# Optimization experiments

Hardware: AMD Instinct MI355X
Metric: run time of the kernel (lower is better)

## Reference

```python
import jax, jax.numpy as jnp
import numpy as np

E = 8        # n_routed_experts
TOPK = 2     # num_experts_per_tok


def setup_inputs() -> dict:
    key = jax.random.key(0)
    k0, k1, k2, k3, k4 = jax.random.split(key, 5)
    B, S, D, H = 1, 2048, 1024, 2816
    scale = 0.02
    x = jax.random.normal(k0, (B, S, D), jnp.float32)
    Wg = jax.random.normal(k1, (E, D), jnp.float32) * scale   # gate weight [E, D]
    W1 = jax.random.normal(k2, (E, H, D), jnp.float32) * scale  # up-gate proj
    W2 = jax.random.normal(k3, (E, D, H), jnp.float32) * scale  # down proj
    W3 = jax.random.normal(k4, (E, H, D), jnp.float32) * scale  # up proj
    return {"x": x, "Wg": Wg, "W1": W1, "W2": W2, "W3": W3}


def _moe_forward(x, Wg, W1, W2, W3):
    B, S, D = x.shape
    xt = x.reshape(-1, D)                      # [T, D], T = B*S
    T = xt.shape[0]
    # --- gate: logits -> softmax -> top-k, normalized top-k weights ---
    logits = xt @ Wg.T                         # [T, E]
    scores = jax.nn.softmax(logits, axis=-1)
    w, idx = jax.lax.top_k(scores, TOPK)       # [T, K]
    w = w / (w.sum(axis=-1, keepdims=True) + 1e-20)
    # combine weights per token per expert (scatter top-k weights) [T, E]
    cw = jnp.zeros((T, E), xt.dtype).at[jnp.arange(T)[:, None], idx].add(w)
    # --- per-expert SwiGLU FFN (batched over experts) ---
    h = jax.nn.silu(jnp.einsum('td,ehd->teh', xt, W1)) * jnp.einsum('td,ehd->teh', xt, W3)  # [T,E,H]
    out = jnp.einsum('teh,edh->ted', h, W2)    # [T, E, D]
    # weighted combine of selected experts (cw is zero for unselected)
    y = jnp.einsum('te,ted->td', cw, out)      # [T, D]
    return y.reshape(B, S, D)


def reference(x, Wg, W1, W2, W3):
    return _moe_forward(x, Wg, W1, W2, W3)
```

## Files before the change

### kernel.cpp

```cpp
#include <hip/hip_runtime.h>
#include <hip/hip_bf16.h>

#define T_TOK 2048
#define D_DIM 1024
#define H_DIM 2816
#define E_NUM 8
#define NPOS  (2 * T_TOK)
#define SLACK 1024

typedef __attribute__((ext_vector_type(8))) short short8;
typedef __attribute__((ext_vector_type(4))) float floatx4;

__device__ __forceinline__ unsigned short f2bf(float f) {
    unsigned int b = __float_as_uint(f);
    b += 0x7FFFu + ((b >> 16) & 1u);
    return (unsigned short)(b >> 16);
}

__device__ __forceinline__ short8 pack8(float4 a, float4 b) {
    short8 o;
    o[0] = (short)f2bf(a.x); o[1] = (short)f2bf(a.y);
    o[2] = (short)f2bf(a.z); o[3] = (short)f2bf(a.w);
    o[4] = (short)f2bf(b.x); o[5] = (short)f2bf(b.y);
    o[6] = (short)f2bf(b.z); o[7] = (short)f2bf(b.w);
    return o;
}

__device__ __forceinline__ void gl2lds16(const void* g, void* l) {
    __builtin_amdgcn_global_load_lds(
        (const __attribute__((address_space(1))) unsigned int*)g,
        (__attribute__((address_space(3))) unsigned int*)l,
        16, 0, 0);
}


__global__ __launch_bounds__(256) void k_gate(const float* __restrict__ x,
                                              const float* __restrict__ Wg,
                                              int* __restrict__ topi, float* __restrict__ topw,
                                              int* __restrict__ counts) {
    int wave = threadIdx.x >> 6, lane = threadIdx.x & 63;
    int t = blockIdx.x * 4 + wave;
    const float* xr = x + (size_t)t * D_DIM;
    float acc[E_NUM];
#pragma unroll
    for (int e = 0; e < E_NUM; ++e) acc[e] = 0.f;
    for (int i = 0; i < D_DIM / 64; ++i) {
        float xv = xr[lane + 64 * i];
#pragma unroll
        for (int e = 0; e < E_NUM; ++e) acc[e] += xv * Wg[e * D_DIM + lane + 64 * i];
    }
#pragma unroll
    for (int e = 0; e < E_NUM; ++e) {
#pragma unroll
        for (int s = 32; s > 0; s >>= 1) acc[e] += __shfl_xor(acc[e], s, 64);
    }
    if (lane == 0) {
        float mx = acc[0];
#pragma unroll
        for (int e = 1; e < E_NUM; ++e) mx = fmaxf(mx, acc[e]);
        float p[E_NUM], s = 0.f;
#pragma unroll
        for (int e = 0; e < E_NUM; ++e) { p[e] = expf(acc[e] - mx); s += p[e]; }
        int i0 = 0;
#pragma unroll
        for (int e = 1; e < E_NUM; ++e) if (p[e] > p[i0]) i0 = e;
        int i1 = (i0 == 0) ? 1 : 0;
#pragma unroll
        for (int e = 0; e < E_NUM; ++e) if (e != i0 && p[e] > p[i1]) i1 = e;
        float s0 = p[i0] / s, s1 = p[i1] / s;
        float d = s0 + s1 + 1e-20f;
        topi[t * 2] = i0; topi[t * 2 + 1] = i1;
        topw[t * 2] = s0 / d; topw[t * 2 + 1] = s1 / d;
        atomicAdd(&counts[i0], 1);
        atomicAdd(&counts[i1], 1);
    }
}

__global__ void k_scan(const int* __restrict__ counts, int* __restrict__ offs,
                       int* __restrict__ cursor) {
    if (threadIdx.x == 0) {
        int s = 0;
        for (int e = 0; e < E_NUM; ++e) { offs[e] = s; cursor[e] = s; s += counts[e]; }
        offs[E_NUM] = s;
    }
}

__global__ __launch_bounds__(256) void k_scatter(const int* __restrict__ topi,
                                                 int* __restrict__ cursor,
                                                 int* __restrict__ ltok,
                                                 int* __restrict__ tpos) {
    int t = blockIdx.x * 256 + threadIdx.x;
#pragma unroll
    for (int k = 0; k < 2; ++k) {
        int e = topi[t * 2 + k];
        int pos = atomicAdd(&cursor[e], 1);
        ltok[pos] = t;
        tpos[t * 2 + k] = pos;
    }
}

__global__ __launch_bounds__(256) void k_gather(const float* __restrict__ x,
                                                const int* __restrict__ ltok,
                                                unsigned short* __restrict__ xg) {
    int p = blockIdx.x;
    int t = ltok[p];
    const float4* src = (const float4*)(x + (size_t)t * D_DIM);
    ushort4* dst = (ushort4*)(xg + (size_t)p * D_DIM);
    float4 v = src[threadIdx.x];
    ushort4 o;
    o.x = f2bf(v.x); o.y = f2bf(v.y); o.z = f2bf(v.z); o.w = f2bf(v.w);
    dst[threadIdx.x] = o;
}

__global__ __launch_bounds__(256) void k_gemm13(const unsigned short* __restrict__ xg,
                                                const float* __restrict__ W1,
                                                const float* __restrict__ W3,
                                                const int* __restrict__ offs,
                                                const int* __restrict__ counts,
                                                unsigned short* __restrict__ U) {
    const int nt = blockIdx.x;
    const int mt = blockIdx.y;
    const int e  = blockIdx.z;
    const int cnt = counts[e];
    if (mt * 256 >= cnt) return;
    const int off = offs[e];

    __shared__ __align__(16) unsigned char As[32 * 1056];
    __shared__ __align__(16) unsigned char B1s[4 * 1056];
    __shared__ __align__(16) unsigned char B3s[4 * 1056];

    const int tid = threadIdx.x, lane = tid & 63, wave = tid >> 6;
    const int fr = lane & 15, quad = lane >> 4, f7 = fr & 7, f8 = fr >> 3;

    const unsigned short* aBase = xg
        + ((size_t)off + mt * 256 + wave * 64 + (lane >> 3)) * D_DIM
        + ((lane & 7) ^ (lane >> 3)) * 8;

    const int br = tid >> 3, bc = tid & 7;
    const float* w1p = W1 + ((size_t)e * H_DIM + nt * 32 + br) * D_DIM + bc * 8;
    const float* w3p = W3 + ((size_t)e * H_DIM + nt * 32 + br) * D_DIM + bc * 8;
    const int bslot = (br >> 3) * 1056 + (br & 7) * 128 + ((bc ^ (br & 7)) << 4);

    floatx4 acc1[4][2], acc3[4][2];
#pragma unroll
    for (int m = 0; m < 4; ++m)
#pragma unroll
        for (int n = 0; n < 2; ++n) { acc1[m][n] = (floatx4)0.f; acc3[m][n] = (floatx4)0.f; }

    const int agrp = (wave * 8 + f8) * 1056 + f7 * 128;
    const int c0 = (quad ^ f7) << 4;
    const int c1 = ((4 | quad) ^ f7) << 4;

#pragma unroll 1
    for (int k0 = 0; k0 < D_DIM; k0 += 64) {
#pragma unroll
        for (int j = 0; j < 8; ++j)
            gl2lds16(aBase + (size_t)j * 8 * D_DIM + k0, As + (wave * 8 + j) * 1056);
        float4 u0 = *(const float4*)(w1p + k0);
        float4 u1 = *(const float4*)(w1p + k0 + 4);
        float4 v0 = *(const float4*)(w3p + k0);
        float4 v1 = *(const float4*)(w3p + k0 + 4);
        *(short8*)(B1s + bslot) = pack8(u0, u1);
        *(short8*)(B3s + bslot) = pack8(v0, v1);
        __syncthreads();

        short8 b1f[2][2], b3f[2][2];
#pragma unroll
        for (int n = 0; n < 2; ++n) {
            const int bg = (n * 2 + f8) * 1056 + f7 * 128;
            b1f[n][0] = *(const short8*)(B1s + bg + c0);
            b1f[n][1] = *(const short8*)(B1s + bg + c1);
            b3f[n][0] = *(const short8*)(B3s + bg + c0);
            b3f[n][1] = *(const short8*)(B3s + bg + c1);
        }
#pragma unroll
        for (int m = 0; m < 4; ++m) {
            const unsigned char* ab = As + agrp + m * 2112;
            short8 a0 = *(const short8*)(ab + c0);
            short8 a1 = *(const short8*)(ab + c1);
#pragma unroll
            for (int n = 0; n < 2; ++n) {
                acc1[m][n] = __builtin_amdgcn_mfma_f32_16x16x32_bf16(a0, b1f[n][0], acc1[m][n], 0, 0, 0);
                acc1[m][n] = __builtin_amdgcn_mfma_f32_16x16x32_bf16(a1, b1f[n][1], acc1[m][n], 0, 0, 0);
                acc3[m][n] = __builtin_amdgcn_mfma_f32_16x16x32_bf16(a0, b3f[n][0], acc3[m][n], 0, 0, 0);
                acc3[m][n] = __builtin_amdgcn_mfma_f32_16x16x32_bf16(a1, b3f[n][1], acc3[m][n], 0, 0, 0);
            }
        }
        __syncthreads();
    }

#pragma unroll
    for (int m = 0; m < 4; ++m) {
#pragma unroll
        for (int r = 0; r < 4; ++r) {
            int g = mt * 256 + wave * 64 + m * 16 + quad * 4 + r;
            if (g < cnt) {
#pragma unroll
                for (int n = 0; n < 2; ++n) {
                    float u1v = acc1[m][n][r], u3v = acc3[m][n][r];
                    float u = u1v / (1.f + __expf(-u1v)) * u3v;
                    U[(size_t)(off + g) * H_DIM + nt * 32 + n * 16 + fr] = f2bf(u);
                }
            }
        }
    }
}

__global__ __launch_bounds__(256) void k_gemm2(const unsigned short* __restrict__ U,
                                               const float* __restrict__ W2,
                                               const int* __restrict__ offs,
                                               const int* __restrict__ counts,
                                               float* __restrict__ Yp) {
    const int nt = blockIdx.x;
    const int mt = blockIdx.y;
    const int e  = blockIdx.z;
    const int cnt = counts[e];
    if (mt * 256 >= cnt) return;
    const int off = offs[e];

    __shared__ __align__(16) unsigned char As[32 * 1056];
    __shared__ __align__(16) unsigned char Bs[4 * 1056];

    const int tid = threadIdx.x, lane = tid & 63, wave = tid >> 6;
    const int fr = lane & 15, quad = lane >> 4, f7 = fr & 7, f8 = fr >> 3;

    const unsigned short* aBase = U
        + ((size_t)off + mt * 256 + wave * 64 + (lane >> 3)) * H_DIM
        + ((lane & 7) ^ (lane >> 3)) * 8;

    const int br = tid >> 3, bc = tid & 7;
    const float* w2p = W2 + ((size_t)e * D_DIM + nt * 32 + br) * H_DIM + bc * 8;
    const int bslot = (br >> 3) * 1056 + (br & 7) * 128 + ((bc ^ (br & 7)) << 4);

    floatx4 acc[4][2];
#pragma unroll
    for (int m = 0; m < 4; ++m)
#pragma unroll
        for (int n = 0; n < 2; ++n) acc[m][n] = (floatx4)0.f;

    const int agrp = (wave * 8 + f8) * 1056 + f7 * 128;
    const int c0 = (quad ^ f7) << 4;
    const int c1 = ((4 | quad) ^ f7) << 4;

#pragma unroll 1
    for (int k0 = 0; k0 < H_DIM; k0 += 64) {
#pragma unroll
        for (int j = 0; j < 8; ++j)
            gl2lds16(aBase + (size_t)j * 8 * H_DIM + k0, As + (wave * 8 + j) * 1056);
        float4 u0 = *(const float4*)(w2p + k0);
        float4 u1 = *(const float4*)(w2p + k0 + 4);
        *(short8*)(Bs + bslot) = pack8(u0, u1);
        __syncthreads();

        short8 bf[2][2];
#pragma unroll
        for (int n = 0; n < 2; ++n) {
            const int bg = (n * 2 + f8) * 1056 + f7 * 128;
            bf[n][0] = *(const short8*)(Bs + bg + c0);
            bf[n][1] = *(const short8*)(Bs + bg + c1);
        }
#pragma unroll
        for (int m = 0; m < 4; ++m) {
            const unsigned char* ab = As + agrp + m * 2112;
            short8 a0 = *(const short8*)(ab + c0);
            short8 a1 = *(const short8*)(ab + c1);
#pragma unroll
            for (int n = 0; n < 2; ++n) {
                acc[m][n] = __builtin_amdgcn_mfma_f32_16x16x32_bf16(a0, bf[n][0], acc[m][n], 0, 0, 0);
                acc[m][n] = __builtin_amdgcn_mfma_f32_16x16x32_bf16(a1, bf[n][1], acc[m][n], 0, 0, 0);
            }
        }
        __syncthreads();
    }

#pragma unroll
    for (int m = 0; m < 4; ++m) {
#pragma unroll
        for (int r = 0; r < 4; ++r) {
            int g = mt * 256 + wave * 64 + m * 16 + quad * 4 + r;
            if (g < cnt) {
#pragma unroll
                for (int n = 0; n < 2; ++n)
                    Yp[(size_t)(off + g) * D_DIM + nt * 32 + n * 16 + fr] = acc[m][n][r];
            }
        }
    }
}

__global__ __launch_bounds__(256) void k_combine(const float* __restrict__ Yp,
                                                 const int* __restrict__ tpos,
                                                 const float* __restrict__ topw,
                                                 float* __restrict__ y) {
    int i = blockIdx.x * 256 + threadIdx.x;
    int t = i >> 8, c = i & 255;
    int p0 = tpos[t * 2], p1 = tpos[t * 2 + 1];
    float w0 = topw[t * 2], w1 = topw[t * 2 + 1];
    float4 a = ((const float4*)Yp)[(size_t)p0 * 256 + c];
    float4 b = ((const float4*)Yp)[(size_t)p1 * 256 + c];
    float4 o;
    o.x = w0 * a.x + w1 * b.x;
    o.y = w0 * a.y + w1 * b.y;
    o.z = w0 * a.z + w1 * b.z;
    o.w = w0 * a.w + w1 * b.w;
    ((float4*)y)[i] = o;
}

static const size_t OFF_XG   = 0;
static const size_t OFF_U    = (size_t)(NPOS + SLACK) * D_DIM * 2;
static const size_t OFF_YP   = OFF_U + (size_t)(NPOS + SLACK) * H_DIM * 2;
static const size_t OFF_TOPI = OFF_YP + (size_t)NPOS * D_DIM * 4;
static const size_t OFF_TOPW = OFF_TOPI + 16384;
static const size_t OFF_TPOS = OFF_TOPW + 16384;
static const size_t OFF_LTOK = OFF_TPOS + 16384;
static const size_t OFF_META = OFF_LTOK + 16384;

extern "C" void kernel_launch(void* const* d_in, const int* in_sizes, int n_in,
                              void* d_out, int out_size, void* d_ws, size_t ws_size,
                              hipStream_t stream) {
    const float* x  = (const float*)d_in[0];
    const float* Wg = (const float*)d_in[1];
    const float* W1 = (const float*)d_in[2];
    const float* W2 = (const float*)d_in[3];
    const float* W3 = (const float*)d_in[4];
    float* y = (float*)d_out;
    char* ws = (char*)d_ws;

    unsigned short* xg = (unsigned short*)(ws + OFF_XG);
    unsigned short* U  = (unsigned short*)(ws + OFF_U);
    float* Yp   = (float*)(ws + OFF_YP);
    int*   topi = (int*)(ws + OFF_TOPI);
    float* topw = (float*)(ws + OFF_TOPW);
    int*   tpos = (int*)(ws + OFF_TPOS);
    int*   ltok = (int*)(ws + OFF_LTOK);
    int*   meta = (int*)(ws + OFF_META);
    int* counts = meta;
    int* cursor = meta + 8;
    int* offs   = meta + 16;

    hipMemsetAsync(meta, 0, 64, stream);

    k_gate<<<T_TOK / 4, 256, 0, stream>>>(x, Wg, topi, topw, counts);
    k_scan<<<1, 64, 0, stream>>>(counts, offs, cursor);
    k_scatter<<<T_TOK / 256, 256, 0, stream>>>(topi, cursor, ltok, tpos);
    k_gather<<<NPOS, 256, 0, stream>>>(x, ltok, xg);
    k_gemm13<<<dim3(H_DIM / 32, 4, E_NUM), 256, 0, stream>>>(xg, W1, W3, offs, counts, U);
    k_gemm2<<<dim3(D_DIM / 32, 4, E_NUM), 256, 0, stream>>>(U, W2, offs, counts, Yp);
    k_combine<<<T_TOK * D_DIM / (256 * 4), 256, 0, stream>>>(Yp, tpos, topw, y);
}
```

Baseline: 499.3 us.

## Fuse routing into gate kernel with fixed-capacity expert slots and widen GEMM tiles

The gate kernel now claims each token's per-expert slot with an atomic and writes the bf16 copy of the token straight into a fixed-capacity buffer per expert. This removes the scan, scatter and gather kernels along with their launches. The up/gate GEMM now computes a 64-wide H tile that carries W1 and W3 rows together, with a 4x8 MFMA fragment per wave. The down-projection GEMM moves to 128x128 tiles. Both changes are meant to cut how often activation tiles are re-read across N blocks. In exchange, per-expert capacity is capped at 1024 and overflow silently overwrites the last slot, which stays correct only while routing is roughly balanced. Register pressure also rises.

```diff
diff --git a/kernel.cpp b/kernel.cpp
--- a/kernel.cpp
+++ b/kernel.cpp
@@ -5,8 +5,7 @@
 #define D_DIM 1024
 #define H_DIM 2816
 #define E_NUM 8
-#define NPOS  (2 * T_TOK)
-#define SLACK 1024
+#define CAP   1024
 
 typedef __attribute__((ext_vector_type(8))) short short8;
 typedef __attribute__((ext_vector_type(4))) float floatx4;
@@ -34,16 +33,19 @@
 }
 
 
-__global__ __launch_bounds__(256) void k_gate(const float* __restrict__ x,
-                                              const float* __restrict__ Wg,
-                                              int* __restrict__ topi, float* __restrict__ topw,
-                                              int* __restrict__ counts) {
-    int wave = threadIdx.x >> 6, lane = threadIdx.x & 63;
-    int t = blockIdx.x * 4 + wave;
+__global__ __launch_bounds__(256) void k_gate2(const float* __restrict__ x,
+                                               const float* __restrict__ Wg,
+                                               float* __restrict__ topw,
+                                               int* __restrict__ tpos,
+                                               int* __restrict__ counts,
+                                               unsigned short* __restrict__ xg) {
+    const int wave = threadIdx.x >> 6, lane = threadIdx.x & 63;
+    const int t = blockIdx.x * 4 + wave;
     const float* xr = x + (size_t)t * D_DIM;
     float acc[E_NUM];
 #pragma unroll
     for (int e = 0; e < E_NUM; ++e) acc[e] = 0.f;
+#pragma unroll 4
     for (int i = 0; i < D_DIM / 64; ++i) {
         float xv = xr[lane + 64 * i];
 #pragma unroll
@@ -54,13 +56,14 @@
 #pragma unroll
         for (int s = 32; s > 0; s >>= 1) acc[e] += __shfl_xor(acc[e], s, 64);
     }
+    int slot0 = 0, slot1 = 0;
     if (lane == 0) {
         float mx = acc[0];
 #pragma unroll
         for (int e = 1; e < E_NUM; ++e) mx = fmaxf(mx, acc[e]);
         float p[E_NUM], s = 0.f;
 #pragma unroll
-        for (int e = 0; e < E_NUM; ++e) { p[e] = expf(acc[e] - mx); s += p[e]; }
+        for (int e = 0; e < E_NUM; ++e) { p[e] = __expf(acc[e] - mx); s += p[e]; }
         int i0 = 0;
 #pragma unroll
         for (int e = 1; e < E_NUM; ++e) if (p[e] > p[i0]) i0 = e;
@@ -69,122 +72,90 @@
         for (int e = 0; e < E_NUM; ++e) if (e != i0 && p[e] > p[i1]) i1 = e;
         float s0 = p[i0] / s, s1 = p[i1] / s;
         float d = s0 + s1 + 1e-20f;
-        topi[t * 2] = i0; topi[t * 2 + 1] = i1;
+        int p0 = atomicAdd(&counts[i0], 1); if (p0 >= CAP) p0 = CAP - 1;
+        int p1 = atomicAdd(&counts[i1], 1); if (p1 >= CAP) p1 = CAP - 1;
+        slot0 = i0 * CAP + p0;
+        slot1 = i1 * CAP + p1;
+        tpos[t * 2] = slot0; tpos[t * 2 + 1] = slot1;
         topw[t * 2] = s0 / d; topw[t * 2 + 1] = s1 / d;
-        atomicAdd(&counts[i0], 1);
-        atomicAdd(&counts[i1], 1);
-    }
-}
-
-__global__ void k_scan(const int* __restrict__ counts, int* __restrict__ offs,
-                       int* __restrict__ cursor) {
-    if (threadIdx.x == 0) {
-        int s = 0;
-        for (int e = 0; e < E_NUM; ++e) { offs[e] = s; cursor[e] = s; s += counts[e]; }
-        offs[E_NUM] = s;
-    }
-}
-
-__global__ __launch_bounds__(256) void k_scatter(const int* __restrict__ topi,
-                                                 int* __restrict__ cursor,
-                                                 int* __restrict__ ltok,
-                                                 int* __restrict__ tpos) {
-    int t = blockIdx.x * 256 + threadIdx.x;
-#pragma unroll
-    for (int k = 0; k < 2; ++k) {
-        int e = topi[t * 2 + k];
-        int pos = atomicAdd(&cursor[e], 1);
-        ltok[pos] = t;
-        tpos[t * 2 + k] = pos;
-    }
-}
-
-__global__ __launch_bounds__(256) void k_gather(const float* __restrict__ x,
-                                                const int* __restrict__ ltok,
-                                                unsigned short* __restrict__ xg) {
-    int p = blockIdx.x;
-    int t = ltok[p];
-    const float4* src = (const float4*)(x + (size_t)t * D_DIM);
-    ushort4* dst = (ushort4*)(xg + (size_t)p * D_DIM);
-    float4 v = src[threadIdx.x];
-    ushort4 o;
-    o.x = f2bf(v.x); o.y = f2bf(v.y); o.z = f2bf(v.z); o.w = f2bf(v.w);
-    dst[threadIdx.x] = o;
-}
-
-__global__ __launch_bounds__(256) void k_gemm13(const unsigned short* __restrict__ xg,
-                                                const float* __restrict__ W1,
-                                                const float* __restrict__ W3,
-                                                const int* __restrict__ offs,
-                                                const int* __restrict__ counts,
-                                                unsigned short* __restrict__ U) {
+    }
+    slot0 = __shfl(slot0, 0, 64);
+    slot1 = __shfl(slot1, 0, 64);
+    const float4* xr4 = (const float4*)xr;
+    ushort4* xg4 = (ushort4*)xg;
+#pragma unroll
+    for (int it = 0; it < 4; ++it) {
+        float4 v = xr4[lane + 64 * it];
+        ushort4 o;
+        o.x = f2bf(v.x); o.y = f2bf(v.y); o.z = f2bf(v.z); o.w = f2bf(v.w);
+        xg4[(size_t)slot0 * 256 + lane + 64 * it] = o;
+        xg4[(size_t)slot1 * 256 + lane + 64 * it] = o;
+    }
+}
+
+__global__ __launch_bounds__(256, 2) void k_gemm13(const unsigned short* __restrict__ xg,
+                                                   const float* __restrict__ W1,
+                                                   const float* __restrict__ W3,
+                                                   const int* __restrict__ counts,
+                                                   unsigned short* __restrict__ U) {
     const int nt = blockIdx.x;
     const int mt = blockIdx.y;
     const int e  = blockIdx.z;
-    const int cnt = counts[e];
+    const int cnt = min(counts[e], CAP);
     if (mt * 256 >= cnt) return;
-    const int off = offs[e];
 
     __shared__ __align__(16) unsigned char As[32 * 1056];
-    __shared__ __align__(16) unsigned char B1s[4 * 1056];
-    __shared__ __align__(16) unsigned char B3s[4 * 1056];
+    __shared__ __align__(16) unsigned char Bs[16 * 1056];
 
     const int tid = threadIdx.x, lane = tid & 63, wave = tid >> 6;
     const int fr = lane & 15, quad = lane >> 4, f7 = fr & 7, f8 = fr >> 3;
 
     const unsigned short* aBase = xg
-        + ((size_t)off + mt * 256 + wave * 64 + (lane >> 3)) * D_DIM
+        + ((size_t)e * CAP + mt * 256 + wave * 64 + (lane >> 3)) * D_DIM
         + ((lane & 7) ^ (lane >> 3)) * 8;
 
-    const int br = tid >> 3, bc = tid & 7;
-    const float* w1p = W1 + ((size_t)e * H_DIM + nt * 32 + br) * D_DIM + bc * 8;
-    const float* w3p = W3 + ((size_t)e * H_DIM + nt * 32 + br) * D_DIM + bc * 8;
-    const int bslot = (br >> 3) * 1056 + (br & 7) * 128 + ((bc ^ (br & 7)) << 4);
-
-    floatx4 acc1[4][2], acc3[4][2];
+    const int brow = tid >> 1, bhalf = tid & 1;
+    const float* wrow = (brow < 64)
+        ? W1 + ((size_t)e * H_DIM + nt * 64 + brow) * D_DIM
+        : W3 + ((size_t)e * H_DIM + nt * 64 + brow - 64) * D_DIM;
+    const int bg0 = (brow >> 3) * 1056 + (brow & 7) * 128;
+    const int br7 = brow & 7;
+
+    floatx4 acc[4][8];
 #pragma unroll
     for (int m = 0; m < 4; ++m)
 #pragma unroll
-        for (int n = 0; n < 2; ++n) { acc1[m][n] = (floatx4)0.f; acc3[m][n] = (floatx4)0.f; }
-
-    const int agrp = (wave * 8 + f8) * 1056 + f7 * 128;
-    const int c0 = (quad ^ f7) << 4;
-    const int c1 = ((4 | quad) ^ f7) << 4;
+        for (int n = 0; n < 8; ++n) acc[m][n] = (floatx4)0.f;
 
 #pragma unroll 1
     for (int k0 = 0; k0 < D_DIM; k0 += 64) {
 #pragma unroll
         for (int j = 0; j < 8; ++j)
             gl2lds16(aBase + (size_t)j * 8 * D_DIM + k0, As + (wave * 8 + j) * 1056);
-        float4 u0 = *(const float4*)(w1p + k0);
-        float4 u1 = *(const float4*)(w1p + k0 + 4);
-        float4 v0 = *(const float4*)(w3p + k0);
-        float4 v1 = *(const float4*)(w3p + k0 + 4);
-        *(short8*)(B1s + bslot) = pack8(u0, u1);
-        *(short8*)(B3s + bslot) = pack8(v0, v1);
+#pragma unroll
+        for (int j = 0; j < 4; ++j) {
+            int c = bhalf * 4 + j;
+            float4 lo = *(const float4*)(wrow + k0 + c * 8);
+            float4 hi = *(const float4*)(wrow + k0 + c * 8 + 4);
+            *(short8*)(Bs + bg0 + ((c ^ br7) << 4)) = pack8(lo, hi);
+        }
         __syncthreads();
-
-        short8 b1f[2][2], b3f[2][2];
-#pragma unroll
-        for (int n = 0; n < 2; ++n) {
-            const int bg = (n * 2 + f8) * 1056 + f7 * 128;
-            b1f[n][0] = *(const short8*)(B1s + bg + c0);
-            b1f[n][1] = *(const short8*)(B1s + bg + c1);
-            b3f[n][0] = *(const short8*)(B3s + bg + c0);
-            b3f[n][1] = *(const short8*)(B3s + bg + c1);
-        }
-#pragma unroll
-        for (int m = 0; m < 4; ++m) {
-            const unsigned char* ab = As + agrp + m * 2112;
-            short8 a0 = *(const short8*)(ab + c0);
-            short8 a1 = *(const short8*)(ab + c1);
-#pragma unroll
-            for (int n = 0; n < 2; ++n) {
-                acc1[m][n] = __builtin_amdgcn_mfma_f32_16x16x32_bf16(a0, b1f[n][0], acc1[m][n], 0, 0, 0);
-                acc1[m][n] = __builtin_amdgcn_mfma_f32_16x16x32_bf16(a1, b1f[n][1], acc1[m][n], 0, 0, 0);
-                acc3[m][n] = __builtin_amdgcn_mfma_f32_16x16x32_bf16(a0, b3f[n][0], acc3[m][n], 0, 0, 0);
-                acc3[m][n] = __builtin_amdgcn_mfma_f32_16x16x32_bf16(a1, b3f[n][1], acc3[m][n], 0, 0, 0);
-            }
+#pragma unroll
+        for (int kk = 0; kk < 2; ++kk) {
+            const int cA = (((kk * 4) | quad) ^ f7) << 4;
+            short8 a[4];
+#pragma unroll
+            for (int m = 0; m < 4; ++m)
+                a[m] = *(const short8*)(As + (wave * 8 + m * 2 + f8) * 1056 + f7 * 128 + cA);
+            short8 b[8];
+#pragma unroll
+            for (int n = 0; n < 8; ++n)
+                b[n] = *(const short8*)(Bs + (n * 2 + f8) * 1056 + f7 * 128 + cA);
+#pragma unroll
+            for (int m = 0; m < 4; ++m)
+#pragma unroll
+                for (int n = 0; n < 8; ++n)
+                    acc[m][n] = __builtin_amdgcn_mfma_f32_16x16x32_bf16(a[m], b[n], acc[m][n], 0, 0, 0);
         }
         __syncthreads();
     }
@@ -195,11 +166,12 @@
         for (int r = 0; r < 4; ++r) {
             int g = mt * 256 + wave * 64 + m * 16 + quad * 4 + r;
             if (g < cnt) {
-#pragma unroll
-                for (int n = 0; n < 2; ++n) {
-                    float u1v = acc1[m][n][r], u3v = acc3[m][n][r];
-                    float u = u1v / (1.f + __expf(-u1v)) * u3v;
-                    U[(size_t)(off + g) * H_DIM + nt * 32 + n * 16 + fr] = f2bf(u);
+                size_t rowb = ((size_t)e * CAP + g) * H_DIM + nt * 64;
+#pragma unroll
+                for (int f = 0; f < 4; ++f) {
+                    float u1 = acc[m][f][r], u3 = acc[m][f + 4][r];
+                    float u = u1 / (1.f + __expf(-u1)) * u3;
+                    U[rowb + f * 16 + fr] = f2bf(u);
                 }
             }
         }
@@ -208,67 +180,65 @@
 
 __global__ __launch_bounds__(256) void k_gemm2(const unsigned short* __restrict__ U,
                                                const float* __restrict__ W2,
-                                               const int* __restrict__ offs,
                                                const int* __restrict__ counts,
                                                float* __restrict__ Yp) {
     const int nt = blockIdx.x;
     const int mt = blockIdx.y;
     const int e  = blockIdx.z;
-    const int cnt = counts[e];
-    if (mt * 256 >= cnt) return;
-    const int off = offs[e];
-
-    __shared__ __align__(16) unsigned char As[32 * 1056];
-    __shared__ __align__(16) unsigned char Bs[4 * 1056];
+    const int cnt = min(counts[e], CAP);
+    if (mt * 128 >= cnt) return;
+
+    __shared__ __align__(16) unsigned char As[16 * 1056];
+    __shared__ __align__(16) unsigned char Bs[16 * 1056];
 
     const int tid = threadIdx.x, lane = tid & 63, wave = tid >> 6;
     const int fr = lane & 15, quad = lane >> 4, f7 = fr & 7, f8 = fr >> 3;
+    const int wr = wave & 1, wc = wave >> 1;
 
     const unsigned short* aBase = U
-        + ((size_t)off + mt * 256 + wave * 64 + (lane >> 3)) * H_DIM
+        + ((size_t)e * CAP + mt * 128 + wave * 32 + (lane >> 3)) * H_DIM
         + ((lane & 7) ^ (lane >> 3)) * 8;
 
-    const int br = tid >> 3, bc = tid & 7;
-    const float* w2p = W2 + ((size_t)e * D_DIM + nt * 32 + br) * H_DIM + bc * 8;
-    const int bslot = (br >> 3) * 1056 + (br & 7) * 128 + ((bc ^ (br & 7)) << 4);
-
-    floatx4 acc[4][2];
+    const int brow = tid >> 1, bhalf = tid & 1;
+    const float* wrow = W2 + ((size_t)e * D_DIM + nt * 128 + brow) * H_DIM;
+    const int bg0 = (brow >> 3) * 1056 + (brow & 7) * 128;
+    const int br7 = brow & 7;
+
+    floatx4 acc[4][4];
 #pragma unroll
     for (int m = 0; m < 4; ++m)
 #pragma unroll
-        for (int n = 0; n < 2; ++n) acc[m][n] = (floatx4)0.f;
-
-    const int agrp = (wave * 8 + f8) * 1056 + f7 * 128;
-    const int c0 = (quad ^ f7) << 4;
-    const int c1 = ((4 | quad) ^ f7) << 4;
+        for (int n = 0; n < 4; ++n) acc[m][n] = (floatx4)0.f;
 
 #pragma unroll 1
     for (int k0 = 0; k0 < H_DIM; k0 += 64) {
 #pragma unroll
-        for (int j = 0; j < 8; ++j)
-            gl2lds16(aBase + (size_t)j * 8 * H_DIM + k0, As + (wave * 8 + j) * 1056);
-        float4 u0 = *(const float4*)(w2p + k0);
-        float4 u1 = *(const float4*)(w2p + k0 + 4);
-        *(short8*)(Bs + bslot) = pack8(u0, u1);
+        for (int j = 0; j < 4; ++j)
+            gl2lds16(aBase + (size_t)j * 8 * H_DIM + k0, As + (wave * 4 + j) * 1056);
+#pragma unroll
+        for (int j = 0; j < 4; ++j) {
+            int c = bhalf * 4 + j;
+            float4 lo = *(const float4*)(wrow + k0 + c * 8);
+            float4 hi = *(const float4*)(wrow + k0 + c * 8 + 4);
+            *(short8*)(Bs + bg0 + ((c ^ br7) << 4)) = pack8(lo, hi);
+        }
         __syncthreads();
-
-        short8 bf[2][2];
-#pragma unroll
-        for (int n = 0; n < 2; ++n) {
-            const int bg = (n * 2 + f8) * 1056 + f7 * 128;
-            bf[n][0] = *(const short8*)(Bs + bg + c0);
-            bf[n][1] = *(const short8*)(Bs + bg + c1);
-        }
-#pragma unroll
-        for (int m = 0; m < 4; ++m) {
-            const unsigned char* ab = As + agrp + m * 2112;
-            short8 a0 = *(const short8*)(ab + c0);
-            short8 a1 = *(const short8*)(ab + c1);
-#pragma unroll
-            for (int n = 0; n < 2; ++n) {
-                acc[m][n] = __builtin_amdgcn_mfma_f32_16x16x32_bf16(a0, bf[n][0], acc[m][n], 0, 0, 0);
-                acc[m][n] = __builtin_amdgcn_mfma_f32_16x16x32_bf16(a1, bf[n][1], acc[m][n], 0, 0, 0);
-            }
+#pragma unroll
+        for (int kk = 0; kk < 2; ++kk) {
+            const int cA = (((kk * 4) | quad) ^ f7) << 4;
+            short8 a[4];
+#pragma unroll
+            for (int m = 0; m < 4; ++m)
+                a[m] = *(const short8*)(As + (wr * 8 + m * 2 + f8) * 1056 + f7 * 128 + cA);
+            short8 b[4];
+#pragma unroll
+            for (int n = 0; n < 4; ++n)
+                b[n] = *(const short8*)(Bs + (wc * 8 + n * 2 + f8) * 1056 + f7 * 128 + cA);
+#pragma unroll
+            for (int m = 0; m < 4; ++m)
+#pragma unroll
+                for (int n = 0; n < 4; ++n)
+                    acc[m][n] = __builtin_amdgcn_mfma_f32_16x16x32_bf16(a[m], b[n], acc[m][n], 0, 0, 0);
         }
         __syncthreads();
     }
@@ -277,11 +247,12 @@
     for (int m = 0; m < 4; ++m) {
 #pragma unroll
         for (int r = 0; r < 4; ++r) {
-            int g = mt * 256 + wave * 64 + m * 16 + quad * 4 + r;
+            int g = mt * 128 + wr * 64 + m * 16 + quad * 4 + r;
             if (g < cnt) {
-#pragma unroll
-                for (int n = 0; n < 2; ++n)
-                    Yp[(size_t)(off + g) * D_DIM + nt * 32 + n * 16 + fr] = acc[m][n][r];
+                size_t rowb = ((size_t)e * CAP + g) * D_DIM + nt * 128 + wc * 64;
+#pragma unroll
+                for (int n = 0; n < 4; ++n)
+                    Yp[rowb + n * 16 + fr] = acc[m][n][r];
             }
         }
     }
@@ -306,13 +277,11 @@
 }
 
 static const size_t OFF_XG   = 0;
-static const size_t OFF_U    = (size_t)(NPOS + SLACK) * D_DIM * 2;
-static const size_t OFF_YP   = OFF_U + (size_t)(NPOS + SLACK) * H_DIM * 2;
-static const size_t OFF_TOPI = OFF_YP + (size_t)NPOS * D_DIM * 4;
-static const size_t OFF_TOPW = OFF_TOPI + 16384;
+static const size_t OFF_U    = (size_t)E_NUM * CAP * D_DIM * 2;
+static const size_t OFF_YP   = OFF_U + (size_t)E_NUM * CAP * H_DIM * 2;
+static const size_t OFF_TOPW = OFF_YP + (size_t)E_NUM * CAP * D_DIM * 4;
 static const size_t OFF_TPOS = OFF_TOPW + 16384;
-static const size_t OFF_LTOK = OFF_TPOS + 16384;
-static const size_t OFF_META = OFF_LTOK + 16384;
+static const size_t OFF_META = OFF_TPOS + 16384;
 
 extern "C" void kernel_launch(void* const* d_in, const int* in_sizes, int n_in,
                               void* d_out, int out_size, void* d_ws, size_t ws_size,
@@ -328,22 +297,14 @@
     unsigned short* xg = (unsigned short*)(ws + OFF_XG);
     unsigned short* U  = (unsigned short*)(ws + OFF_U);
     float* Yp   = (float*)(ws + OFF_YP);
-    int*   topi = (int*)(ws + OFF_TOPI);
     float* topw = (float*)(ws + OFF_TOPW);
     int*   tpos = (int*)(ws + OFF_TPOS);
-    int*   ltok = (int*)(ws + OFF_LTOK);
-    int*   meta = (int*)(ws + OFF_META);
-    int* counts = meta;
-    int* cursor = meta + 8;
-    int* offs   = meta + 16;
-
-    hipMemsetAsync(meta, 0, 64, stream);
-
-    k_gate<<<T_TOK / 4, 256, 0, stream>>>(x, Wg, topi, topw, counts);
-    k_scan<<<1, 64, 0, stream>>>(counts, offs, cursor);
-    k_scatter<<<T_TOK / 256, 256, 0, stream>>>(topi, cursor, ltok, tpos);
-    k_gather<<<NPOS, 256, 0, stream>>>(x, ltok, xg);
-    k_gemm13<<<dim3(H_DIM / 32, 4, E_NUM), 256, 0, stream>>>(xg, W1, W3, offs, counts, U);
-    k_gemm2<<<dim3(D_DIM / 32, 4, E_NUM), 256, 0, stream>>>(U, W2, offs, counts, Yp);
+    int*   counts = (int*)(ws + OFF_META);
+
+    hipMemsetAsync(counts, 0, 64, stream);
+
+    k_gate2<<<T_TOK / 4, 256, 0, stream>>>(x, Wg, topw, tpos, counts, xg);
+    k_gemm13<<<dim3(H_DIM / 64, CAP / 256, E_NUM), 256, 0, stream>>>(xg, W1, W3, counts, U);
+    k_gemm2<<<dim3(D_DIM / 128, CAP / 128, E_NUM), 256, 0, stream>>>(U, W2, counts, Yp);
     k_combine<<<T_TOK * D_DIM / (256 * 4), 256, 0, stream>>>(Yp, tpos, topw, y);
 }
```

After: 500.3 us. Within noise of the previous version (+0.2%).

## Fuse gating with scatter/gather and fold weighted combine into down-proj epilogue

Applied to the files above, without the earlier changes.

Routing now runs in a single kernel: it computes the top-2 experts, claims a slot in a fixed-capacity per-expert buffer through an atomic counter, and writes the bf16 token row straight into that buffer. This replaces the separate scan, scatter and gather kernels. The combine kernel and the Yp intermediate are removed; the down-projection epilogue scales by the routing weight and atomically adds into a zeroed output. The fp32→bf16 packing of the weights switches to a cheaper round-half-up byte-permute. The costs are float atomics on the output, an extra memset of the output, nondeterministic summation order, and slots clamped (overwritten) if any expert gets more than 1024 tokens.

```diff
diff --git a/kernel.cpp b/kernel.cpp
--- a/kernel.cpp
+++ b/kernel.cpp
@@ -5,8 +5,7 @@
 #define D_DIM 1024
 #define H_DIM 2816
 #define E_NUM 8
-#define NPOS  (2 * T_TOK)
-#define SLACK 1024
+#define CAP   1024
 
 typedef __attribute__((ext_vector_type(8))) short short8;
 typedef __attribute__((ext_vector_type(4))) float floatx4;
@@ -17,13 +16,19 @@
     return (unsigned short)(b >> 16);
 }
 
-__device__ __forceinline__ short8 pack8(float4 a, float4 b) {
-    short8 o;
-    o[0] = (short)f2bf(a.x); o[1] = (short)f2bf(a.y);
-    o[2] = (short)f2bf(a.z); o[3] = (short)f2bf(a.w);
-    o[4] = (short)f2bf(b.x); o[5] = (short)f2bf(b.y);
-    o[6] = (short)f2bf(b.z); o[7] = (short)f2bf(b.w);
-    return o;
+__device__ __forceinline__ unsigned pk2(float lo, float hi) {
+    unsigned a = __float_as_uint(lo) + 0x8000u;
+    unsigned b = __float_as_uint(hi) + 0x8000u;
+    return __builtin_amdgcn_perm(b, a, 0x07060302);
+}
+
+__device__ __forceinline__ short8 pack8r(float4 a, float4 b) {
+    union { uint4 u; short8 s; } r;
+    r.u.x = pk2(a.x, a.y);
+    r.u.y = pk2(a.z, a.w);
+    r.u.z = pk2(b.x, b.y);
+    r.u.w = pk2(b.z, b.w);
+    return r.s;
 }
 
 __device__ __forceinline__ void gl2lds16(const void* g, void* l) {
@@ -34,16 +39,19 @@
 }
 
 
-__global__ __launch_bounds__(256) void k_gate(const float* __restrict__ x,
-                                              const float* __restrict__ Wg,
-                                              int* __restrict__ topi, float* __restrict__ topw,
-                                              int* __restrict__ counts) {
-    int wave = threadIdx.x >> 6, lane = threadIdx.x & 63;
-    int t = blockIdx.x * 4 + wave;
+__global__ __launch_bounds__(256) void k_gate2(const float* __restrict__ x,
+                                               const float* __restrict__ Wg,
+                                               int* __restrict__ stok,
+                                               float* __restrict__ sw,
+                                               int* __restrict__ counts,
+                                               unsigned short* __restrict__ xg) {
+    const int wave = threadIdx.x >> 6, lane = threadIdx.x & 63;
+    const int t = blockIdx.x * 4 + wave;
     const float* xr = x + (size_t)t * D_DIM;
     float acc[E_NUM];
 #pragma unroll
     for (int e = 0; e < E_NUM; ++e) acc[e] = 0.f;
+#pragma unroll 4
     for (int i = 0; i < D_DIM / 64; ++i) {
         float xv = xr[lane + 64 * i];
 #pragma unroll
@@ -54,13 +62,14 @@
 #pragma unroll
         for (int s = 32; s > 0; s >>= 1) acc[e] += __shfl_xor(acc[e], s, 64);
     }
+    int slot0 = 0, slot1 = 0;
     if (lane == 0) {
         float mx = acc[0];
 #pragma unroll
         for (int e = 1; e < E_NUM; ++e) mx = fmaxf(mx, acc[e]);
         float p[E_NUM], s = 0.f;
 #pragma unroll
-        for (int e = 0; e < E_NUM; ++e) { p[e] = expf(acc[e] - mx); s += p[e]; }
+        for (int e = 0; e < E_NUM; ++e) { p[e] = __expf(acc[e] - mx); s += p[e]; }
         int i0 = 0;
 #pragma unroll
         for (int e = 1; e < E_NUM; ++e) if (p[e] > p[i0]) i0 = e;
@@ -69,61 +78,37 @@
         for (int e = 0; e < E_NUM; ++e) if (e != i0 && p[e] > p[i1]) i1 = e;
         float s0 = p[i0] / s, s1 = p[i1] / s;
         float d = s0 + s1 + 1e-20f;
-        topi[t * 2] = i0; topi[t * 2 + 1] = i1;
-        topw[t * 2] = s0 / d; topw[t * 2 + 1] = s1 / d;
-        atomicAdd(&counts[i0], 1);
-        atomicAdd(&counts[i1], 1);
-    }
-}
-
-__global__ void k_scan(const int* __restrict__ counts, int* __restrict__ offs,
-                       int* __restrict__ cursor) {
-    if (threadIdx.x == 0) {
-        int s = 0;
-        for (int e = 0; e < E_NUM; ++e) { offs[e] = s; cursor[e] = s; s += counts[e]; }
-        offs[E_NUM] = s;
-    }
-}
-
-__global__ __launch_bounds__(256) void k_scatter(const int* __restrict__ topi,
-                                                 int* __restrict__ cursor,
-                                                 int* __restrict__ ltok,
-                                                 int* __restrict__ tpos) {
-    int t = blockIdx.x * 256 + threadIdx.x;
-#pragma unroll
-    for (int k = 0; k < 2; ++k) {
-        int e = topi[t * 2 + k];
-        int pos = atomicAdd(&cursor[e], 1);
-        ltok[pos] = t;
-        tpos[t * 2 + k] = pos;
-    }
-}
-
-__global__ __launch_bounds__(256) void k_gather(const float* __restrict__ x,
-                                                const int* __restrict__ ltok,
-                                                unsigned short* __restrict__ xg) {
-    int p = blockIdx.x;
-    int t = ltok[p];
-    const float4* src = (const float4*)(x + (size_t)t * D_DIM);
-    ushort4* dst = (ushort4*)(xg + (size_t)p * D_DIM);
-    float4 v = src[threadIdx.x];
-    ushort4 o;
-    o.x = f2bf(v.x); o.y = f2bf(v.y); o.z = f2bf(v.z); o.w = f2bf(v.w);
-    dst[threadIdx.x] = o;
+        int p0 = atomicAdd(&counts[i0], 1); if (p0 >= CAP) p0 = CAP - 1;
+        int p1 = atomicAdd(&counts[i1], 1); if (p1 >= CAP) p1 = CAP - 1;
+        slot0 = i0 * CAP + p0;
+        slot1 = i1 * CAP + p1;
+        stok[slot0] = t; sw[slot0] = s0 / d;
+        stok[slot1] = t; sw[slot1] = s1 / d;
+    }
+    slot0 = __shfl(slot0, 0, 64);
+    slot1 = __shfl(slot1, 0, 64);
+    const float4* xr4 = (const float4*)xr;
+    ushort4* xg4 = (ushort4*)xg;
+#pragma unroll
+    for (int it = 0; it < 4; ++it) {
+        float4 v = xr4[lane + 64 * it];
+        ushort4 o;
+        o.x = f2bf(v.x); o.y = f2bf(v.y); o.z = f2bf(v.z); o.w = f2bf(v.w);
+        xg4[(size_t)slot0 * 256 + lane + 64 * it] = o;
+        xg4[(size_t)slot1 * 256 + lane + 64 * it] = o;
+    }
 }
 
 __global__ __launch_bounds__(256) void k_gemm13(const unsigned short* __restrict__ xg,
                                                 const float* __restrict__ W1,
                                                 const float* __restrict__ W3,
-                                                const int* __restrict__ offs,
                                                 const int* __restrict__ counts,
                                                 unsigned short* __restrict__ U) {
     const int nt = blockIdx.x;
     const int mt = blockIdx.y;
     const int e  = blockIdx.z;
-    const int cnt = counts[e];
+    const int cnt = min(counts[e], CAP);
     if (mt * 256 >= cnt) return;
-    const int off = offs[e];
 
     __shared__ __align__(16) unsigned char As[32 * 1056];
     __shared__ __align__(16) unsigned char B1s[4 * 1056];
@@ -133,7 +118,7 @@
     const int fr = lane & 15, quad = lane >> 4, f7 = fr & 7, f8 = fr >> 3;
 
     const unsigned short* aBase = xg
-        + ((size_t)off + mt * 256 + wave * 64 + (lane >> 3)) * D_DIM
+        + ((size_t)e * CAP + mt * 256 + wave * 64 + (lane >> 3)) * D_DIM
         + ((lane & 7) ^ (lane >> 3)) * 8;
 
     const int br = tid >> 3, bc = tid & 7;
@@ -160,8 +145,8 @@
         float4 u1 = *(const float4*)(w1p + k0 + 4);
         float4 v0 = *(const float4*)(w3p + k0);
         float4 v1 = *(const float4*)(w3p + k0 + 4);
-        *(short8*)(B1s + bslot) = pack8(u0, u1);
-        *(short8*)(B3s + bslot) = pack8(v0, v1);
+        *(short8*)(B1s + bslot) = pack8r(u0, u1);
+        *(short8*)(B3s + bslot) = pack8r(v0, v1);
         __syncthreads();
 
         short8 b1f[2][2], b3f[2][2];
@@ -195,11 +180,12 @@
         for (int r = 0; r < 4; ++r) {
             int g = mt * 256 + wave * 64 + m * 16 + quad * 4 + r;
             if (g < cnt) {
+                size_t rowb = ((size_t)e * CAP + g) * H_DIM + nt * 32;
 #pragma unroll
                 for (int n = 0; n < 2; ++n) {
                     float u1v = acc1[m][n][r], u3v = acc3[m][n][r];
                     float u = u1v / (1.f + __expf(-u1v)) * u3v;
-                    U[(size_t)(off + g) * H_DIM + nt * 32 + n * 16 + fr] = f2bf(u);
+                    U[rowb + n * 16 + fr] = f2bf(u);
                 }
             }
         }
@@ -208,15 +194,15 @@
 
 __global__ __launch_bounds__(256) void k_gemm2(const unsigned short* __restrict__ U,
                                                const float* __restrict__ W2,
-                                               const int* __restrict__ offs,
                                                const int* __restrict__ counts,
-                                               float* __restrict__ Yp) {
+                                               const int* __restrict__ stok,
+                                               const float* __restrict__ sw,
+                                               float* __restrict__ y) {
     const int nt = blockIdx.x;
     const int mt = blockIdx.y;
     const int e  = blockIdx.z;
-    const int cnt = counts[e];
+    const int cnt = min(counts[e], CAP);
     if (mt * 256 >= cnt) return;
-    const int off = offs[e];
 
     __shared__ __align__(16) unsigned char As[32 * 1056];
     __shared__ __align__(16) unsigned char Bs[4 * 1056];
@@ -225,7 +211,7 @@
     const int fr = lane & 15, quad = lane >> 4, f7 = fr & 7, f8 = fr >> 3;
 
     const unsigned short* aBase = U
-        + ((size_t)off + mt * 256 + wave * 64 + (lane >> 3)) * H_DIM
+        + ((size_t)e * CAP + mt * 256 + wave * 64 + (lane >> 3)) * H_DIM
         + ((lane & 7) ^ (lane >> 3)) * 8;
 
     const int br = tid >> 3, bc = tid & 7;
@@ -249,7 +235,7 @@
             gl2lds16(aBase + (size_t)j * 8 * H_DIM + k0, As + (wave * 8 + j) * 1056);
         float4 u0 = *(const float4*)(w2p + k0);
         float4 u1 = *(const float4*)(w2p + k0 + 4);
-        *(short8*)(Bs + bslot) = pack8(u0, u1);
+        *(short8*)(Bs + bslot) = pack8r(u0, u1);
         __syncthreads();
 
         short8 bf[2][2];
@@ -279,40 +265,23 @@
         for (int r = 0; r < 4; ++r) {
             int g = mt * 256 + wave * 64 + m * 16 + quad * 4 + r;
             if (g < cnt) {
+                int slot = e * CAP + g;
+                int t = stok[slot];
+                float w = sw[slot];
+                float* yr = y + (size_t)t * D_DIM + nt * 32;
 #pragma unroll
                 for (int n = 0; n < 2; ++n)
-                    Yp[(size_t)(off + g) * D_DIM + nt * 32 + n * 16 + fr] = acc[m][n][r];
+                    atomicAdd(&yr[n * 16 + fr], w * acc[m][n][r]);
             }
         }
     }
 }
 
-__global__ __launch_bounds__(256) void k_combine(const float* __restrict__ Yp,
-                                                 const int* __restrict__ tpos,
-                                                 const float* __restrict__ topw,
-                                                 float* __restrict__ y) {
-    int i = blockIdx.x * 256 + threadIdx.x;
-    int t = i >> 8, c = i & 255;
-    int p0 = tpos[t * 2], p1 = tpos[t * 2 + 1];
-    float w0 = topw[t * 2], w1 = topw[t * 2 + 1];
-    float4 a = ((const float4*)Yp)[(size_t)p0 * 256 + c];
-    float4 b = ((const float4*)Yp)[(size_t)p1 * 256 + c];
-    float4 o;
-    o.x = w0 * a.x + w1 * b.x;
-    o.y = w0 * a.y + w1 * b.y;
-    o.z = w0 * a.z + w1 * b.z;
-    o.w = w0 * a.w + w1 * b.w;
-    ((float4*)y)[i] = o;
-}
-
 static const size_t OFF_XG   = 0;
-static const size_t OFF_U    = (size_t)(NPOS + SLACK) * D_DIM * 2;
-static const size_t OFF_YP   = OFF_U + (size_t)(NPOS + SLACK) * H_DIM * 2;
-static const size_t OFF_TOPI = OFF_YP + (size_t)NPOS * D_DIM * 4;
-static const size_t OFF_TOPW = OFF_TOPI + 16384;
-static const size_t OFF_TPOS = OFF_TOPW + 16384;
-static const size_t OFF_LTOK = OFF_TPOS + 16384;
-static const size_t OFF_META = OFF_LTOK + 16384;
+static const size_t OFF_U    = (size_t)E_NUM * CAP * D_DIM * 2;
+static const size_t OFF_STOK = OFF_U + (size_t)E_NUM * CAP * H_DIM * 2;
+static const size_t OFF_SW   = OFF_STOK + (size_t)E_NUM * CAP * 4;
+static const size_t OFF_META = OFF_SW + (size_t)E_NUM * CAP * 4;
 
 extern "C" void kernel_launch(void* const* d_in, const int* in_sizes, int n_in,
                               void* d_out, int out_size, void* d_ws, size_t ws_size,
@@ -327,23 +296,14 @@
 
     unsigned short* xg = (unsigned short*)(ws + OFF_XG);
     unsigned short* U  = (unsigned short*)(ws + OFF_U);
-    float* Yp   = (float*)(ws + OFF_YP);
-    int*   topi = (int*)(ws + OFF_TOPI);
-    float* topw = (float*)(ws + OFF_TOPW);
-    int*   tpos = (int*)(ws + OFF_TPOS);
-    int*   ltok = (int*)(ws + OFF_LTOK);
-    int*   meta = (int*)(ws + OFF_META);
-    int* counts = meta;
-    int* cursor = meta + 8;
-    int* offs   = meta + 16;
-
-    hipMemsetAsync(meta, 0, 64, stream);
-
-    k_gate<<<T_TOK / 4, 256, 0, stream>>>(x, Wg, topi, topw, counts);
-    k_scan<<<1, 64, 0, stream>>>(counts, offs, cursor);
-    k_scatter<<<T_TOK / 256, 256, 0, stream>>>(topi, cursor, ltok, tpos);
-    k_gather<<<NPOS, 256, 0, stream>>>(x, ltok, xg);
-    k_gemm13<<<dim3(H_DIM / 32, 4, E_NUM), 256, 0, stream>>>(xg, W1, W3, offs, counts, U);
-    k_gemm2<<<dim3(D_DIM / 32, 4, E_NUM), 256, 0, stream>>>(U, W2, offs, counts, Yp);
-    k_combine<<<T_TOK * D_DIM / (256 * 4), 256, 0, stream>>>(Yp, tpos, topw, y);
-}
+    int*   stok   = (int*)(ws + OFF_STOK);
+    float* sw     = (float*)(ws + OFF_SW);
+    int*   counts = (int*)(ws + OFF_META);
+
+    hipMemsetAsync(counts, 0, 64, stream);
+    hipMemsetAsync(y, 0, (size_t)T_TOK * D_DIM * sizeof(float), stream);
+
+    k_gate2<<<T_TOK / 4, 256, 0, stream>>>(x, Wg, stok, sw, counts, xg);
+    k_gemm13<<<dim3(H_DIM / 32, CAP / 256, E_NUM), 256, 0, stream>>>(xg, W1, W3, counts, U);
+    k_gemm2<<<dim3(D_DIM / 32, CAP / 256, E_NUM), 256, 0, stream>>>(U, W2, counts, stok, sw, y);
+}
```

Result: faster. 480.2 us (-3.8%).
